# Performance work log

Measured on AMD Instinct MI355X. Metric: run time of the kernel, lower is better.

Reference implementation:

```python
import jax, jax.numpy as jnp
import numpy as np

MODEL_DIM = 1024
NUM_HEADS = 16
HEAD_DIM = MODEL_DIM // NUM_HEADS
EPS = 1e-12
CHUNK = 128  # chunk size for the linear-attention recurrence


def setup_inputs() -> dict:
    key = jax.random.key(0)
    kx, kq, kk, kv, ko = jax.random.split(key, 5)
    b, l = 4, 4096
    x = jax.random.normal(kx, (b, l, MODEL_DIM), dtype=jnp.float32)
    # nn.Linear weights, init std=0.02, no bias; torch Linear computes x @ W.T
    Wq = 0.02 * jax.random.normal(kq, (MODEL_DIM, MODEL_DIM), dtype=jnp.float32)
    Wk = 0.02 * jax.random.normal(kk, (MODEL_DIM, MODEL_DIM), dtype=jnp.float32)
    Wv = 0.02 * jax.random.normal(kv, (MODEL_DIM, MODEL_DIM), dtype=jnp.float32)
    Wo = 0.02 * jax.random.normal(ko, (MODEL_DIM, MODEL_DIM), dtype=jnp.float32)
    return {"x": x, "Wq": Wq, "Wk": Wk, "Wv": Wv, "Wo": Wo}


def _pos_elu(t):
    # feature_map = F.elu(x) + 1
    return jax.nn.elu(t) + 1.0


def _linear_attention(q, k, v):
    # q,k,v: (b,h,l,d) with feature map already applied.
    # Causal linear attention: out_t = (q_t . sum_{s<=t} k_s v_s^T) / (q_t . sum_{s<=t} k_s) + EPS
    # Chunked recurrence over the (d,d) KV state avoids the (b,h,l,d,d) cumsum.
    b, h, l, d = q.shape
    nc = l // CHUNK
    qc = jnp.moveaxis(q.reshape(b, h, nc, CHUNK, d), 2, 0)  # (nc,b,h,C,d)
    kc = jnp.moveaxis(k.reshape(b, h, nc, CHUNK, d), 2, 0)
    vc = jnp.moveaxis(v.reshape(b, h, nc, CHUNK, d), 2, 0)
    mask = jnp.tril(jnp.ones((CHUNK, CHUNK), dtype=q.dtype))  # causal within chunk

    def step(carry, inp):
        S, z = carry  # S:(b,h,d,d) running sum k v^T; z:(b,h,d) running sum k
        qb, kb, vb = inp  # (b,h,C,d)
        scores = jnp.einsum('bhcd,bhsd->bhcs', qb, kb) * mask  # (b,h,C,C)
        num = jnp.einsum('bhcd,bhde->bhce', qb, S) + jnp.einsum('bhcs,bhse->bhce', scores, vb)
        den = jnp.einsum('bhcd,bhd->bhc', qb, z) + scores.sum(-1)  # (b,h,C)
        out = num / den[..., None] + EPS  # NOTE: eps added after division, as in source
        S = S + jnp.einsum('bhsd,bhse->bhde', kb, vb)
        z = z + kb.sum(axis=2)
        return (S, z), out

    S0 = jnp.zeros((b, h, d, d), dtype=q.dtype)
    z0 = jnp.zeros((b, h, d), dtype=q.dtype)
    _, outs = jax.lax.scan(step, (S0, z0), (qc, kc, vc))  # (nc,b,h,C,d)
    # -> (b, l, h, d)
    return jnp.moveaxis(outs, 0, 1).transpose(0, 3, 1, 2, 4).reshape(b, h * 0 + l // l, 0, 0) if False else outs


def reference(x, Wq, Wk, Wv, Wo):
    b, l, D = x.shape
    h, d = NUM_HEADS, HEAD_DIM
    # projections (torch Linear: x @ W.T), split heads -> (b,h,l,d)
    q = (x @ Wq.T).reshape(b, l, h, d).transpose(0, 2, 1, 3)
    k = (x @ Wk.T).reshape(b, l, h, d).transpose(0, 2, 1, 3)
    v = (x @ Wv.T).reshape(b, l, h, d).transpose(0, 2, 1, 3)
    q = _pos_elu(q)
    k = _pos_elu(k)
    outs = _linear_attention(q, k, v)  # (nc,b,h,C,d)
    nc = l // CHUNK
    # (nc,b,h,C,d) -> (b,nc,C,h,d) -> (b,l,D)  (matches transpose(1,2).view in torch)
    attn = outs.transpose(1, 0, 3, 2, 4).reshape(b, l, D)
    return attn @ Wo.T
```

## Files before the change

kernel.cpp:

```cpp
#include <hip/hip_runtime.h>
#include <stdint.h>

typedef float f32x4 __attribute__((ext_vector_type(4)));
typedef __bf16 bf16x8 __attribute__((ext_vector_type(8)));
typedef unsigned short u16x8 __attribute__((ext_vector_type(8)));

#define DEV __device__ __forceinline__

DEV unsigned short f2bf(float f) {
  unsigned int u = __float_as_uint(f);
  unsigned int r = (u + 0x7FFFu + ((u >> 16) & 1u)) >> 16;
  return (unsigned short)r;
}
DEV float b2f(unsigned short h) { return __uint_as_float(((unsigned int)h) << 16); }

DEV void gload16(const void* g, void* l) {
  __builtin_amdgcn_global_load_lds((__attribute__((address_space(1))) void*)(g),
                                   (__attribute__((address_space(3))) void*)(l), 16, 0, 0);
}

__global__ void cast_all(const float* __restrict__ x, const float* __restrict__ Wq,
                         const float* __restrict__ Wk, const float* __restrict__ Wv,
                         const float* __restrict__ Wo, unsigned short* __restrict__ xbf,
                         unsigned short* __restrict__ wqkv, unsigned short* __restrict__ wo) {
  int i = blockIdx.x * 256 + threadIdx.x;
  const float* src;
  unsigned short* dst;
  int j;
  if (i < 2097152) {
    src = x; dst = xbf; j = i;
  } else {
    int k = i - 2097152;
    int sel = k >> 17; j = k & 131071;
    src = (sel == 0) ? Wq : (sel == 1) ? Wk : (sel == 2) ? Wv : Wo;
    dst = (sel < 3) ? (wqkv + (size_t)sel * 1048576) : wo;
  }
  const float4* p = (const float4*)src + (size_t)j * 2;
  float4 a = p[0], b = p[1];
  u16x8 o;
  o[0] = f2bf(a.x); o[1] = f2bf(a.y); o[2] = f2bf(a.z); o[3] = f2bf(a.w);
  o[4] = f2bf(b.x); o[5] = f2bf(b.y); o[6] = f2bf(b.z); o[7] = f2bf(b.w);
  ((u16x8*)dst)[j] = o;
}

template<int MODE>
__global__ __launch_bounds__(256, 2) void gemm_bt(
    const unsigned short* __restrict__ A, const unsigned short* __restrict__ Bw,
    void* __restrict__ out0, unsigned short* __restrict__ qp,
    unsigned short* __restrict__ kp, unsigned short* __restrict__ vp,
    int K, int N, int nTn)
{
  __shared__ unsigned short sA[128 * 64];
  __shared__ unsigned short sB[128 * 64];
  int t = threadIdx.x, w = t >> 6, lane = t & 63, fr = lane & 15, fq = lane >> 4;
  int bid = blockIdx.x;
  int bm = bid / nTn, bn = bid % nTn;
  int wm = w >> 1, wn = w & 1;

  f32x4 acc[4][4];
  f32x4 z4 = {0.f, 0.f, 0.f, 0.f};
#pragma unroll
  for (int mi = 0; mi < 4; ++mi)
#pragma unroll
    for (int ni = 0; ni < 4; ++ni) acc[mi][ni] = z4;

  for (int k0 = 0; k0 < K; k0 += 64) {
#pragma unroll
    for (int i = 0; i < 4; ++i) {
      int p = (i * 4 + w) * 64 + lane;
      int r = p >> 3;
      int c8 = (p & 7) ^ (r & 7);
      gload16(A + (size_t)(bm * 128 + r) * K + k0 + c8 * 8, &sA[(i * 4 + w) * 512]);
      gload16(Bw + (size_t)(bn * 128 + r) * K + k0 + c8 * 8, &sB[(i * 4 + w) * 512]);
    }
    __syncthreads();
#pragma unroll
    for (int ks = 0; ks < 2; ++ks) {
      bf16x8 af[4], bg[4];
#pragma unroll
      for (int mi = 0; mi < 4; ++mi) {
        int r = wm * 64 + mi * 16 + fr;
        int c8 = (ks * 4 + fq) ^ (r & 7);
        af[mi] = *(const bf16x8*)&sA[(r * 8 + c8) * 8];
      }
#pragma unroll
      for (int ni = 0; ni < 4; ++ni) {
        int r = wn * 64 + ni * 16 + fr;
        int c8 = (ks * 4 + fq) ^ (r & 7);
        bg[ni] = *(const bf16x8*)&sB[(r * 8 + c8) * 8];
      }
#pragma unroll
      for (int mi = 0; mi < 4; ++mi)
#pragma unroll
        for (int ni = 0; ni < 4; ++ni)
          acc[mi][ni] = __builtin_amdgcn_mfma_f32_16x16x32_bf16(af[mi], bg[ni], acc[mi][ni], 0, 0, 0);
    }
    __syncthreads();
  }

  if (MODE == 0) {
    float* O = (float*)out0;
#pragma unroll
    for (int mi = 0; mi < 4; ++mi)
#pragma unroll
      for (int ni = 0; ni < 4; ++ni)
#pragma unroll
        for (int j = 0; j < 4; ++j) {
          int m = bm * 128 + wm * 64 + mi * 16 + fq * 4 + j;
          int n = bn * 128 + wn * 64 + ni * 16 + fr;
          O[(size_t)m * N + n] = acc[mi][ni][j];
        }
  } else {
    int tsel = (bn * 128) >> 10;
    unsigned short* base = (tsel == 0) ? qp : ((tsel == 1) ? kp : vp);
#pragma unroll
    for (int mi = 0; mi < 4; ++mi)
#pragma unroll
      for (int ni = 0; ni < 4; ++ni)
#pragma unroll
        for (int j = 0; j < 4; ++j) {
          int m = bm * 128 + wm * 64 + mi * 16 + fq * 4 + j;
          int n = bn * 128 + wn * 64 + ni * 16 + fr;
          int col1 = n & 1023;
          int h = col1 >> 6, d = col1 & 63;
          int b = m >> 12, l = m & 4095;
          float v = acc[mi][ni][j];
          if (tsel < 2) v = (v > 0.f) ? (v + 1.f) : __expf(v);
          base[(((size_t)(b * 16 + h)) * 4096 + l) * 64 + d] = f2bf(v);
        }
  }
}

__global__ __launch_bounds__(256) void chunk_state(
    const unsigned short* __restrict__ kb, const unsigned short* __restrict__ vb,
    unsigned short* __restrict__ Spref, float* __restrict__ zbuf)
{
  __shared__ unsigned short kT[64 * 136];
  __shared__ unsigned short vT[64 * 136];
  int t = threadIdx.x, w = t >> 6, lane = t & 63, fr = lane & 15, fq = lane >> 4;
  int bh = blockIdx.x >> 5, c = blockIdx.x & 31;
  size_t base = ((size_t)bh * 4096 + (size_t)c * 128) * 64;

  int s = t >> 1, d0 = (t & 1) * 32;
  const unsigned short* kpp = kb + base + (size_t)s * 64 + d0;
  const unsigned short* vpp = vb + base + (size_t)s * 64 + d0;
#pragma unroll
  for (int i = 0; i < 4; ++i) {
    u16x8 kr = *(const u16x8*)(kpp + i * 8);
    u16x8 vr = *(const u16x8*)(vpp + i * 8);
#pragma unroll
    for (int j = 0; j < 8; ++j) {
      int d = d0 + i * 8 + j;
      kT[d * 136 + s] = kr[j];
      vT[d * 136 + s] = vr[j];
    }
  }
  __syncthreads();

  f32x4 acc[4];
  f32x4 z4 = {0.f, 0.f, 0.f, 0.f};
#pragma unroll
  for (int n = 0; n < 4; ++n) acc[n] = z4;
#pragma unroll
  for (int ks = 0; ks < 4; ++ks) {
    bf16x8 av = *(const bf16x8*)&vT[(w * 16 + fr) * 136 + ks * 32 + fq * 8];
#pragma unroll
    for (int n = 0; n < 4; ++n) {
      bf16x8 bk = *(const bf16x8*)&kT[(n * 16 + fr) * 136 + ks * 32 + fq * 8];
      acc[n] = __builtin_amdgcn_mfma_f32_16x16x32_bf16(av, bk, acc[n], 0, 0, 0);
    }
  }
  size_t ob = ((size_t)bh * 32 + c) * 4096;
#pragma unroll
  for (int n = 0; n < 4; ++n)
#pragma unroll
    for (int j = 0; j < 4; ++j) {
      int e = w * 16 + fq * 4 + j, dd = n * 16 + fr;
      Spref[ob + (size_t)e * 64 + dd] = f2bf(acc[n][j]);
    }
  if (t < 64) {
    float z = 0.f;
#pragma unroll
    for (int i = 0; i < 16; ++i) {
      u16x8 kr = *(const u16x8*)&kT[t * 136 + i * 8];
#pragma unroll
      for (int j = 0; j < 8; ++j) z += b2f(kr[j]);
    }
    zbuf[((size_t)bh * 32 + c) * 64 + t] = z;
  }
}

__global__ __launch_bounds__(256) void scan_all(
    unsigned short* __restrict__ Spref, const float* __restrict__ zbuf,
    float* __restrict__ zpref)
{
  if (blockIdx.x < 512) {
    int idx = blockIdx.x * 256 + threadIdx.x;
    int bh = idx >> 11, i = idx & 2047;
    unsigned int* p32 = (unsigned int*)Spref;
    size_t base = (size_t)bh * 32 * 2048 + i;
    float r0 = 0.f, r1 = 0.f;
#pragma unroll
    for (int c = 0; c < 32; ++c) {
      unsigned int v = p32[base + (size_t)c * 2048];
      float v0 = b2f((unsigned short)(v & 0xFFFFu));
      float v1 = b2f((unsigned short)(v >> 16));
      p32[base + (size_t)c * 2048] =
          (unsigned int)f2bf(r0) | ((unsigned int)f2bf(r1) << 16);
      r0 += v0; r1 += v1;
    }
  } else {
    int idx = (blockIdx.x - 512) * 256 + threadIdx.x;
    size_t base = (size_t)(idx >> 6) * 32 * 64 + (idx & 63);
    float run = 0.f;
#pragma unroll
    for (int c = 0; c < 32; ++c) {
      float v = zbuf[base + c * 64];
      zpref[base + c * 64] = run;
      run += v;
    }
  }
}

__global__ __launch_bounds__(256, 2) void chunk_out(
    const unsigned short* __restrict__ qb, const unsigned short* __restrict__ kb,
    const unsigned short* __restrict__ vb, const unsigned short* __restrict__ Spref,
    const float* __restrict__ zpref, unsigned short* __restrict__ attn)
{
  __shared__ unsigned short sq[128 * 64];
  __shared__ unsigned short skv[128 * 64];
  __shared__ unsigned short ss[128 * 128];
  __shared__ unsigned short sS[80 * 64];
  int t = threadIdx.x, w = t >> 6, lane = t & 63, fr = lane & 15, fq = lane >> 4;
  int bh = blockIdx.x >> 5, c = blockIdx.x & 31;
  size_t qkbase = ((size_t)bh * 4096 + (size_t)c * 128) * 64;
  size_t sbase = ((size_t)bh * 32 + c) * 4096;

#pragma unroll
  for (int i = 0; i < 4; ++i) {
    int p = (i * 4 + w) * 64 + lane;
    int r = p >> 3;
    int c8 = (p & 7) ^ (r & 7);
    gload16(qb + qkbase + (size_t)r * 64 + c8 * 8, &sq[(i * 4 + w) * 512]);
    gload16(kb + qkbase + (size_t)r * 64 + c8 * 8, &skv[(i * 4 + w) * 512]);
  }
#pragma unroll
  for (int i = 0; i < 2; ++i) {
    int p = (i * 4 + w) * 64 + lane;
    int e = p >> 3;
    int c8 = (p & 7) ^ (e & 7);
    gload16(Spref + sbase + (size_t)e * 64 + c8 * 8, &sS[(i * 4 + w) * 512]);
  }

  u16x8 vreg[4];
#pragma unroll
  for (int i = 0; i < 4; ++i)
    vreg[i] = *(const u16x8*)(vb + qkbase + (size_t)(t * 4 + i) * 8);

  if (t < 64) sS[64 * 64 + t] = f2bf(zpref[((size_t)bh * 32 + c) * 64 + t]);
  {
    unsigned int* zz = (unsigned int*)&sS[65 * 64];
    for (int i = t; i < 480; i += 256) zz[i] = 0u;
  }
  __syncthreads();

  int rowbase = w * 32;
  bf16x8 aq[2][2];
#pragma unroll
  for (int mi = 0; mi < 2; ++mi)
#pragma unroll
    for (int kt = 0; kt < 2; ++kt) {
      int r = rowbase + mi * 16 + fr;
      int c8 = (kt * 4 + fq) ^ (r & 7);
      aq[mi][kt] = *(const bf16x8*)&sq[(r * 8 + c8) * 8];
    }

  f32x4 accsT[2][8];
  f32x4 z4 = {0.f, 0.f, 0.f, 0.f};
#pragma unroll
  for (int mi = 0; mi < 2; ++mi)
#pragma unroll
    for (int ni = 0; ni < 8; ++ni) accsT[mi][ni] = z4;

#pragma unroll
  for (int ni = 0; ni < 8; ++ni)
#pragma unroll
    for (int kt = 0; kt < 2; ++kt) {
      int r = ni * 16 + fr;
      int c8 = (kt * 4 + fq) ^ (r & 7);
      bf16x8 bk = *(const bf16x8*)&skv[(r * 8 + c8) * 8];
      accsT[0][ni] = __builtin_amdgcn_mfma_f32_16x16x32_bf16(bk, aq[0][kt], accsT[0][ni], 0, 0, 0);
      accsT[1][ni] = __builtin_amdgcn_mfma_f32_16x16x32_bf16(bk, aq[1][kt], accsT[1][ni], 0, 0, 0);
    }

  float rs[2];
#pragma unroll
  for (int mi = 0; mi < 2; ++mi) {
    int m16 = mi * 16 + fr;
    float sum = 0.f;
#pragma unroll
    for (int ni = 0; ni < 8; ++ni)
#pragma unroll
      for (int j = 0; j < 4; ++j) {
        int s = ni * 16 + fq * 4 + j - rowbase;
        float v = (s <= m16) ? accsT[mi][ni][j] : 0.f;
        accsT[mi][ni][j] = v;
        sum += v;
      }
    sum += __shfl_xor(sum, 16, 64);
    sum += __shfl_xor(sum, 32, 64);
    rs[mi] = sum;
  }
  __syncthreads();

#pragma unroll
  for (int i = 0; i < 4; ++i) {
    int p = t * 4 + i, s = p >> 3, e0g = (p & 7) * 8;
#pragma unroll
    for (int j = 0; j < 8; ++j) {
      int e = e0g + j;
      skv[(e * 16 + ((s >> 3) ^ (e & 15))) * 8 + (s & 7)] = vreg[i][j];
    }
  }
#pragma unroll
  for (int mi = 0; mi < 2; ++mi) {
    int m = rowbase + mi * 16 + fr;
#pragma unroll
    for (int ni = 0; ni < 8; ++ni)
#pragma unroll
      for (int p = 0; p < 2; ++p) {
        unsigned int pk = (unsigned int)f2bf(accsT[mi][ni][2 * p]) |
                          ((unsigned int)f2bf(accsT[mi][ni][2 * p + 1]) << 16);
        int chunk = (2 * ni + (fq >> 1)) ^ (m & 15);
        *(unsigned int*)&ss[m * 128 + chunk * 8 + (fq & 1) * 4 + 2 * p] = pk;
      }
  }
  __syncthreads();

  f32x4 acco[2][4];
  f32x4 accd[2];
#pragma unroll
  for (int mi = 0; mi < 2; ++mi) {
    accd[mi] = z4;
#pragma unroll
    for (int ni = 0; ni < 4; ++ni) acco[mi][ni] = z4;
  }
#pragma unroll
  for (int kt = 0; kt < 2; ++kt) {
#pragma unroll
    for (int ni = 0; ni < 4; ++ni) {
      int r = ni * 16 + fr;
      int c8 = (kt * 4 + fq) ^ (r & 7);
      bf16x8 bS = *(const bf16x8*)&sS[(r * 8 + c8) * 8];
      acco[0][ni] = __builtin_amdgcn_mfma_f32_16x16x32_bf16(aq[0][kt], bS, acco[0][ni], 0, 0, 0);
      acco[1][ni] = __builtin_amdgcn_mfma_f32_16x16x32_bf16(aq[1][kt], bS, acco[1][ni], 0, 0, 0);
    }
    {
      int r = 64 + fr;
      int c8 = (kt * 4 + fq) ^ (r & 7);
      bf16x8 bz = *(const bf16x8*)&sS[(r * 8 + c8) * 8];
      accd[0] = __builtin_amdgcn_mfma_f32_16x16x32_bf16(aq[0][kt], bz, accd[0], 0, 0, 0);
      accd[1] = __builtin_amdgcn_mfma_f32_16x16x32_bf16(aq[1][kt], bz, accd[1], 0, 0, 0);
    }
  }
#pragma unroll
  for (int kt = 0; kt < 4; ++kt) {
    bf16x8 am[2];
#pragma unroll
    for (int mi = 0; mi < 2; ++mi) {
      int r = rowbase + mi * 16 + fr;
      int c8 = (kt * 4 + fq) ^ (r & 15);
      am[mi] = *(const bf16x8*)&ss[(r * 16 + c8) * 8];
    }
#pragma unroll
    for (int ni = 0; ni < 4; ++ni) {
      int r = ni * 16 + fr;
      int c8 = (kt * 4 + fq) ^ (r & 15);
      bf16x8 bv = *(const bf16x8*)&skv[(r * 16 + c8) * 8];
      acco[0][ni] = __builtin_amdgcn_mfma_f32_16x16x32_bf16(am[0], bv, acco[0][ni], 0, 0, 0);
      acco[1][ni] = __builtin_amdgcn_mfma_f32_16x16x32_bf16(am[1], bv, acco[1][ni], 0, 0, 0);
    }
  }

  int b = bh >> 4, h = bh & 15;
#pragma unroll
  for (int mi = 0; mi < 2; ++mi)
#pragma unroll
    for (int j = 0; j < 4; ++j) {
      float rsj = __shfl(rs[mi], fq * 4 + j, 64);
      float den = __shfl(accd[mi][j], (lane & 48), 64) + rsj;
      float rden = 1.f / den;
      int m = rowbase + mi * 16 + fq * 4 + j;
      size_t rowoff = ((size_t)b * 4096 + (size_t)c * 128 + m) * 1024 + h * 64;
#pragma unroll
      for (int ni = 0; ni < 4; ++ni) {
        int e = ni * 16 + fr;
        float o = acco[mi][ni][j] * rden + 1e-12f;
        attn[rowoff + e] = f2bf(o);
      }
    }
}

extern "C" void kernel_launch(void* const* d_in, const int* in_sizes, int n_in,
                              void* d_out, int out_size, void* d_ws, size_t ws_size,
                              hipStream_t stream) {
  (void)in_sizes; (void)n_in; (void)out_size; (void)ws_size;
  const float* x = (const float*)d_in[0];
  const float* Wq = (const float*)d_in[1];
  const float* Wk = (const float*)d_in[2];
  const float* Wv = (const float*)d_in[3];
  const float* Wo = (const float*)d_in[4];
  char* ws = (char*)d_ws;
  unsigned short* xbf  = (unsigned short*)(ws + 0);
  unsigned short* wqkv = (unsigned short*)(ws + 33554432);
  unsigned short* wo   = (unsigned short*)(ws + 39845888);
  unsigned short* q    = (unsigned short*)(ws + 41943040);
  unsigned short* k    = (unsigned short*)(ws + 75497472);
  unsigned short* v    = (unsigned short*)(ws + 109051904);
  unsigned short* attn = (unsigned short*)(ws + 142606336);
  unsigned short* Spref= (unsigned short*)(ws + 176160768);
  float* zbuf          = (float*)(ws + 192937984);
  float* zpref         = (float*)(ws + 193462272);

  cast_all<<<10240, 256, 0, stream>>>(x, Wq, Wk, Wv, Wo, xbf, wqkv, wo);
  gemm_bt<1><<<3072, 256, 0, stream>>>(xbf, wqkv, nullptr, q, k, v, 1024, 3072, 24);
  chunk_state<<<2048, 256, 0, stream>>>(k, v, Spref, zbuf);
  scan_all<<<528, 256, 0, stream>>>(Spref, zbuf, zpref);
  chunk_out<<<2048, 256, 0, stream>>>(q, k, v, Spref, zpref, attn);
  gemm_bt<0><<<1024, 256, 0, stream>>>(attn, wo, d_out, nullptr, nullptr, nullptr, 1024, 1024, 8);
}
```

Baseline: 225.5 us.

## Stage GEMM and attention epilogues through LDS for 16-byte coalesced stores

The QKV GEMM epilogue and the attention output epilogue now write bf16 results into a swizzled LDS tile first, then copy them out as 16-byte vectors so each head row is stored contiguously. Before, each lane wrote a scattered 2-byte value to global memory. The bf16 conversion also switches from a manual round-to-nearest-even to the compiler's native cast. The cost is an extra barrier, and the attention kernel reuses the sq buffer, so it depends on that buffer being free and large enough at that point.

```diff
diff --git a/kernel.cpp b/kernel.cpp
--- a/kernel.cpp
+++ b/kernel.cpp
@@ -8,9 +8,10 @@
 #define DEV __device__ __forceinline__
 
 DEV unsigned short f2bf(float f) {
-  unsigned int u = __float_as_uint(f);
-  unsigned int r = (u + 0x7FFFu + ((u >> 16) & 1u)) >> 16;
-  return (unsigned short)r;
+  __bf16 h = (__bf16)f;
+  unsigned short u;
+  __builtin_memcpy(&u, &h, 2);
+  return u;
 }
 DEV float b2f(unsigned short h) { return __uint_as_float(((unsigned int)h) << 16); }
 
@@ -50,8 +51,9 @@
     unsigned short* __restrict__ kp, unsigned short* __restrict__ vp,
     int K, int N, int nTn)
 {
-  __shared__ unsigned short sA[128 * 64];
-  __shared__ unsigned short sB[128 * 64];
+  __shared__ unsigned short sAB[2 * 128 * 64];
+  unsigned short* sA = sAB;
+  unsigned short* sB = sAB + 8192;
   int t = threadIdx.x, w = t >> 6, lane = t & 63, fr = lane & 15, fq = lane >> 4;
   int bid = blockIdx.x;
   int bm = bid / nTn, bn = bid % nTn;
@@ -119,15 +121,30 @@
       for (int ni = 0; ni < 4; ++ni)
 #pragma unroll
         for (int j = 0; j < 4; ++j) {
-          int m = bm * 128 + wm * 64 + mi * 16 + fq * 4 + j;
-          int n = bn * 128 + wn * 64 + ni * 16 + fr;
-          int col1 = n & 1023;
-          int h = col1 >> 6, d = col1 & 63;
-          int b = m >> 12, l = m & 4095;
+          int ml = wm * 64 + mi * 16 + fq * 4 + j;
+          int nl = wn * 64 + ni * 16 + fr;
           float v = acc[mi][ni][j];
           if (tsel < 2) v = (v > 0.f) ? (v + 1.f) : __expf(v);
-          base[(((size_t)(b * 16 + h)) * 4096 + l) * 64 + d] = f2bf(v);
+          int cidx = nl >> 3;
+          int key = (ml ^ (ml >> 3)) & 7;
+          int cs = (cidx & 8) | ((cidx ^ key) & 7);
+          sAB[ml * 128 + cs * 8 + (nl & 7)] = f2bf(v);
         }
+    __syncthreads();
+    int hbase = ((bn * 128) & 1023) >> 6;
+#pragma unroll
+    for (int i = 0; i < 8; ++i) {
+      int cc = i * 256 + t;
+      int row = cc >> 4, c8 = cc & 15;
+      int key = (row ^ (row >> 3)) & 7;
+      int cs = (c8 & 8) | ((c8 ^ key) & 7);
+      u16x8 val = *(const u16x8*)&sAB[row * 128 + cs * 8];
+      int mg = bm * 128 + row;
+      int b = mg >> 12, l = mg & 4095;
+      int hh = hbase + (c8 >> 3);
+      int d = (c8 & 7) * 8;
+      *(u16x8*)(base + (((size_t)(b * 16 + hh)) * 4096 + l) * 64 + d) = val;
+    }
   }
 }
 
@@ -391,14 +408,27 @@
       float den = __shfl(accd[mi][j], (lane & 48), 64) + rsj;
       float rden = 1.f / den;
       int m = rowbase + mi * 16 + fq * 4 + j;
-      size_t rowoff = ((size_t)b * 4096 + (size_t)c * 128 + m) * 1024 + h * 64;
+      int key = (m ^ (m >> 3)) & 7;
 #pragma unroll
       for (int ni = 0; ni < 4; ++ni) {
         int e = ni * 16 + fr;
-        float o = acco[mi][ni][j] * rden + 1e-12f;
-        attn[rowoff + e] = f2bf(o);
+        float o = acco[ni >> 31][ni][j];
+        o = acco[0][ni][j];
+        (void)o;
+        float ov = ((mi == 0) ? acco[0][ni][j] : acco[1][ni][j]) * rden + 1e-12f;
+        int cidx = e >> 3;
+        sq[m * 64 + ((cidx ^ key) & 7) * 8 + (e & 7)] = f2bf(ov);
       }
     }
+  __syncthreads();
+#pragma unroll
+  for (int i = 0; i < 4; ++i) {
+    int cc = i * 256 + t;
+    int row = cc >> 3, c8 = cc & 7;
+    int key = (row ^ (row >> 3)) & 7;
+    u16x8 val = *(const u16x8*)&sq[row * 64 + ((c8 ^ key) & 7) * 8];
+    *(u16x8*)(attn + ((size_t)b * 4096 + (size_t)c * 128 + row) * 1024 + h * 64 + c8 * 8) = val;
+  }
 }
 
 extern "C" void kernel_launch(void* const* d_in, const int* in_sizes, int n_in,
```

Result: slower. 231.3 us (+2.6%).
